# Optimization experiments

Measured on AMD Instinct MI355X. Metric: run time of the kernel, lower is better.

Reference implementation:

```python
import jax, jax.numpy as jnp
from jax import lax
import numpy as np

PARAM_SPECS = [
    ("w1", (16, 15, 5, 5)), ("b1", (16,)),
    ("w2", (32, 16, 3, 3)), ("b2", (32,)),
    ("w3", (32, 32, 3, 3)), ("b3", (32,)),
    ("w4", (32, 32, 3, 3)), ("b4", (32,)),
    ("w5", (64, 32, 3, 3)), ("b5", (64,)),
    ("w6", (32, 96, 3, 3)), ("b6", (32,)),
    ("w7", (32, 64, 3, 3)), ("b7", (32,)),
    ("w8", (32, 64, 3, 3)), ("b8", (32,)),
    ("w9", (64, 48, 3, 3)), ("b9", (64,)),
    ("wi", (16, 15, 3, 3)), ("bi", (16,)),
    ("wo", (3, 16, 3, 3)), ("bo", (3,)),
]


def conv2d(x, w, b, pad):
    y = lax.conv_general_dilated(x, w, (1, 1), [(pad, pad), (pad, pad)],
                                 dimension_numbers=("NCHW", "OIHW", "NCHW"))
    return y + b[None, :, None, None]


def maxpool2(x):
    return lax.reduce_window(x, -jnp.inf, lax.max, (1, 1, 2, 2), (1, 1, 2, 2), "VALID")


def upsample(x, hw):
    # bilinear, half-pixel centers == torch align_corners=False
    B, C = x.shape[:2]
    return jax.image.resize(x, (B, C, hw[0], hw[1]), method="bilinear")


def dcnn(img, p):
    x1 = jax.nn.relu(conv2d(img, p["w1"], p["b1"], 2))
    x2 = jax.nn.relu(conv2d(maxpool2(x1), p["w2"], p["b2"], 1))
    x3 = jax.nn.relu(conv2d(maxpool2(x2), p["w3"], p["b3"], 1))
    x4 = jax.nn.relu(conv2d(maxpool2(x3), p["w4"], p["b4"], 1))
    x5 = jax.nn.relu(conv2d(maxpool2(x4), p["w5"], p["b5"], 1))
    x6 = jax.nn.relu(conv2d(jnp.concatenate([upsample(x5, x4.shape[-2:]), x4], 1), p["w6"], p["b6"], 1))
    x7 = jax.nn.relu(conv2d(jnp.concatenate([upsample(x6, x3.shape[-2:]), x3], 1), p["w7"], p["b7"], 1))
    x8 = jax.nn.relu(conv2d(jnp.concatenate([upsample(x7, x2.shape[-2:]), x2], 1), p["w8"], p["b8"], 1))
    x9 = conv2d(jnp.concatenate([upsample(x8, x1.shape[-2:]), x1], 1), p["w9"], p["b9"], 1)
    return x9


def lrnn_op(X, P, axis, flip):
    # h_k = (1-P_k)*X_k + P_k*h_{k-1}, scanned along `axis`.
    # For reverse directions the torch code stacks hidden states in scan
    # order (spatially flipped) -> flip inputs, scan forward, keep order.
    if flip:
        X = jnp.flip(X, axis)
        P = jnp.flip(P, axis)
    xs = jnp.moveaxis(X, axis, 0)  # [L, B, 16, n]
    ps = jnp.moveaxis(P, axis, 0)

    def step(h, xp):
        x, p = xp
        h = (1.0 - p) * x + p * h
        return h, h

    h0 = jnp.zeros_like(xs[0])
    _, ys = lax.scan(step, h0, (xs, ps))
    return jnp.moveaxis(ys, 0, axis)


def lrnn_layer(x_in, fm):
    dirs = [(0, 3, False), (0, 3, True), (16, 2, False), (16, 2, True),
            (32, 3, False), (32, 3, True), (48, 2, False), (48, 2, True)]
    outs = [lrnn_op(x_in, fm[:, c:c + 16], axis, flip) for (c, axis, flip) in dirs]
    return jnp.max(jnp.stack(outs, axis=1), axis=1)


def setup_inputs() -> dict:
    key = jax.random.key(0)
    ks = jax.random.split(key, len(PARAM_SPECS) + 1)
    inp = {"img": jax.random.normal(ks[0], (8, 15, 256, 256), jnp.float32)}
    for i, (name, shape) in enumerate(PARAM_SPECS):
        inp[name] = jax.random.normal(ks[i + 1], shape, jnp.float32) * 0.05
    return inp


def reference(img, w1, b1, w2, b2, w3, b3, w4, b4, w5, b5, w6, b6, w7, b7,
              w8, b8, w9, b9, wi, bi, wo, bo):
    p = dict(w1=w1, b1=b1, w2=w2, b2=b2, w3=w3, b3=b3, w4=w4, b4=b4, w5=w5,
             b5=b5, w6=w6, b6=b6, w7=w7, b7=b7, w8=w8, b8=b8, w9=w9, b9=b9)
    fm = jnp.tanh(dcnn(img, p))          # [B,64,H,W]
    x_in = conv2d(img, wi, bi, 1)         # [B,16,H,W]
    out = lrnn_layer(x_in, fm)            # [B,16,H,W]
    return jax.nn.sigmoid(conv2d(out, wo, bo, 1))  # [B,3,H,W]
```

## Files before the change

### kernel.cpp

```cpp
#include <hip/hip_runtime.h>
#include <math.h>

typedef __attribute__((ext_vector_type(8)))  short bf16x8;
typedef __attribute__((ext_vector_type(8)))  unsigned short u16x8;
typedef __attribute__((ext_vector_type(16))) float f32x16;

__device__ __forceinline__ unsigned short f2bf(float f) {
    unsigned u = __float_as_uint(f);
    unsigned r = (u + 0x7FFFu + ((u >> 16) & 1u)) >> 16;
    return (unsigned short)r;
}
__device__ __forceinline__ float bf2f(unsigned short h) {
    return __uint_as_float(((unsigned)h) << 16);
}
__device__ __forceinline__ unsigned pack2(unsigned short a, unsigned short b) {
    return (unsigned)a | ((unsigned)b << 16);
}
__device__ __forceinline__ float fast_tanh(float x) {
    float e = __expf(2.f * x);
    return 1.f - 2.f / (e + 1.f);
}

__device__ __forceinline__ void bilin_setup(int y, int x, int Hi, int Wi,
                                            int& i00, int& i01, int& i10, int& i11,
                                            float& wy, float& wx)
{
    float fy = 0.5f * y - 0.25f;
    float fx = 0.5f * x - 0.25f;
    float y0f = floorf(fy), x0f = floorf(fx);
    wy = fy - y0f; wx = fx - x0f;
    int yA = (int)y0f, xA = (int)x0f;
    int yB = yA + 1, xB = xA + 1;
    yA = yA < 0 ? 0 : (yA > Hi - 1 ? Hi - 1 : yA);
    yB = yB < 0 ? 0 : (yB > Hi - 1 ? Hi - 1 : yB);
    xA = xA < 0 ? 0 : (xA > Wi - 1 ? Wi - 1 : xA);
    xB = xB < 0 ? 0 : (xB > Wi - 1 ? Wi - 1 : xB);
    i00 = yA * Wi + xA; i01 = yA * Wi + xB;
    i10 = yB * Wi + xA; i11 = yB * Wi + xB;
}

__global__ void upcat_nhwc2(const unsigned short* __restrict__ up,
                            const unsigned short* __restrict__ skip,
                            unsigned short* __restrict__ dst,
                            int C1, int C2, int H, int W)
{
    int C8 = (C1 + C2) >> 3;
    int idx = blockIdx.x * 256 + threadIdx.x;
    int total = 8 * H * W * C8;
    if (idx >= total) return;
    int g = idx % C8;
    int p = idx / C8;
    int x = p % W;
    int y = (p / W) % H;
    int b = p / (W * H);
    u16x8 r;
    if (g < (C1 >> 3)) {
        int Hi = H >> 1, Wi = W >> 1;
        int i00, i01, i10, i11; float wy, wx;
        bilin_setup(y, x, Hi, Wi, i00, i01, i10, i11, wy, wx);
        const unsigned short* sb = up + (size_t)b * Hi * Wi * C1 + g * 8;
        u16x8 v00 = *(const u16x8*)(sb + (size_t)i00 * C1);
        u16x8 v01 = *(const u16x8*)(sb + (size_t)i01 * C1);
        u16x8 v10 = *(const u16x8*)(sb + (size_t)i10 * C1);
        u16x8 v11 = *(const u16x8*)(sb + (size_t)i11 * C1);
        float w00 = (1.f - wy) * (1.f - wx), w01 = (1.f - wy) * wx;
        float w10 = wy * (1.f - wx),         w11 = wy * wx;
#pragma unroll
        for (int j = 0; j < 8; ++j)
            r[j] = f2bf(w00 * bf2f(v00[j]) + w01 * bf2f(v01[j]) +
                        w10 * bf2f(v10[j]) + w11 * bf2f(v11[j]));
    } else {
        r = *(const u16x8*)(skip + ((size_t)(b * H + y) * W + x) * C2 + (g - (C1 >> 3)) * 8);
    }
    *(u16x8*)(dst + (((size_t)(b * H + y) * W + x) * (C1 + C2) + g * 8)) = r;
}

__global__ void upx8_kernel(const unsigned short* __restrict__ x8t,
                            unsigned short* __restrict__ x8u)
{
    int idx = blockIdx.x * 256 + threadIdx.x;
    if (idx >= 8 * 256 * 256 * 4) return;
    int g = idx & 3;
    int p = idx >> 2;
    int x = p & 255, y = (p >> 8) & 255, b = p >> 16;
    int i00, i01, i10, i11; float wy, wx;
    bilin_setup(y, x, 128, 128, i00, i01, i10, i11, wy, wx);
    const unsigned short* sb = x8t + (size_t)b * 128 * 128 * 32 + g * 8;
    u16x8 v00 = *(const u16x8*)(sb + (size_t)i00 * 32);
    u16x8 v01 = *(const u16x8*)(sb + (size_t)i01 * 32);
    u16x8 v10 = *(const u16x8*)(sb + (size_t)i10 * 32);
    u16x8 v11 = *(const u16x8*)(sb + (size_t)i11 * 32);
    float w00 = (1.f - wy) * (1.f - wx), w01 = (1.f - wy) * wx;
    float w10 = wy * (1.f - wx),         w11 = wy * wx;
    u16x8 r;
#pragma unroll
    for (int j = 0; j < 8; ++j)
        r[j] = f2bf(w00 * bf2f(v00[j]) + w01 * bf2f(v01[j]) +
                    w10 * bf2f(v10[j]) + w11 * bf2f(v11[j]));
    *(u16x8*)(x8u + (size_t)idx * 8) = r;
}

__global__ void imgT_bf16(const float* __restrict__ img, unsigned short* __restrict__ dst)
{
    int idx = blockIdx.x * 256 + threadIdx.x;
    if (idx >= 8 * 256 * 256) return;
    int x = idx & 255, y = (idx >> 8) & 255, b = idx >> 16;
    unsigned short v[16];
#pragma unroll
    for (int c = 0; c < 15; ++c)
        v[c] = f2bf(img[(size_t)(b * 15 + c) * 65536 + y * 256 + x]);
    v[15] = 0;
    uint4 lo = make_uint4(pack2(v[0], v[1]), pack2(v[2], v[3]), pack2(v[4], v[5]), pack2(v[6], v[7]));
    uint4 hi = make_uint4(pack2(v[8], v[9]), pack2(v[10], v[11]), pack2(v[12], v[13]), pack2(v[14], v[15]));
    *(uint4*)(dst + (size_t)idx * 16)     = lo;
    *(uint4*)(dst + (size_t)idx * 16 + 8) = hi;
}

__device__ __forceinline__ void pack33(const float* __restrict__ w,
                                       unsigned short* __restrict__ dst,
                                       int i, int Cin, int Cout)
{
    int KST = Cin >> 4, MT = Cout >> 5;
    int j = i & 7;
    int lane = (i >> 3) & 63;
    int t = i >> 9;
    int mt = t % MT; t /= MT;
    int kst = t % KST;
    int s = t / KST;
    int oc = mt * 32 + (lane & 31);
    int ci = kst * 16 + (lane >> 5) * 8 + j;
    dst[i] = f2bf(w[(oc * Cin + ci) * 9 + s]);
}

__global__ void wprep_mega(const float* __restrict__ w9, const float* __restrict__ w8,
                           const float* __restrict__ w1, const float* __restrict__ wi,
                           const float* __restrict__ wo, const float* __restrict__ w2,
                           const float* __restrict__ w3, const float* __restrict__ w4,
                           const float* __restrict__ w5, const float* __restrict__ w6,
                           const float* __restrict__ w7,
                           unsigned short* __restrict__ wpk9, unsigned short* __restrict__ wpk8,
                           unsigned short* __restrict__ wpk1, unsigned short* __restrict__ wpki,
                           unsigned short* __restrict__ wpko, unsigned short* __restrict__ wpk2,
                           unsigned short* __restrict__ wpk3, unsigned short* __restrict__ wpk4,
                           unsigned short* __restrict__ wpk5, unsigned short* __restrict__ wpk6,
                           unsigned short* __restrict__ wpk7)
{
    int idx = blockIdx.x * 256 + threadIdx.x;
    if (idx < 27648)       pack33(w9, wpk9, idx, 48, 64);
    else if (idx < 46080)  pack33(w8, wpk8, idx - 27648, 64, 32);
    else if (idx < 58880) {
        int i = idx - 46080;
        int j = i & 7;
        int lane = (i >> 3) & 63;
        int s = i >> 9;
        int oc = lane & 31;
        int ci = (lane >> 5) * 8 + j;
        float v = 0.f;
        if (oc < 16 && ci < 15) v = w1[((oc * 15 + ci) * 5 + s / 5) * 5 + s % 5];
        wpk1[i] = f2bf(v);
    } else if (idx < 63488) {
        int i = idx - 58880;
        int j = i & 7;
        int lane = (i >> 3) & 63;
        int s = i >> 9;
        int oc = lane & 31;
        int ci = (lane >> 5) * 8 + j;
        float v = 0.f;
        if (oc < 16 && ci < 15) v = wi[((oc * 15 + ci) * 3 + s / 3) * 3 + s % 3];
        wpki[i] = f2bf(v);
    } else if (idx < 68096) {
        int i = idx - 63488;
        int j = i & 7;
        int lane = (i >> 3) & 63;
        int s = i >> 9;
        int oc = lane & 31;
        int ci = (lane >> 5) * 8 + j;
        float v = 0.f;
        if (oc < 3) v = wo[((oc * 16 + ci) * 3 + s / 3) * 3 + s % 3];
        wpko[i] = f2bf(v);
    }
    else if (idx < 72704)  pack33(w2, wpk2, idx - 68096, 16, 32);
    else if (idx < 81920)  pack33(w3, wpk3, idx - 72704, 32, 32);
    else if (idx < 91136)  pack33(w4, wpk4, idx - 81920, 32, 32);
    else if (idx < 109568) pack33(w5, wpk5, idx - 91136, 32, 64);
    else if (idx < 137216) pack33(w6, wpk6, idx - 109568, 96, 32);
    else if (idx < 155648) pack33(w7, wpk7, idx - 137216, 64, 32);
}

template<int CIN, int COUT, int H, int W, int ROWS, int POOL>
__global__ __launch_bounds__(256)
void convN_mfma(const unsigned short* __restrict__ in,
                const unsigned short* __restrict__ wpk,
                const float* __restrict__ bias,
                unsigned short* __restrict__ out)
{
    constexpr int G = CIN / 8;
    constexpr int KST = CIN / 16;
    constexpr int MT = COUT / 32;
    constexpr int TR = ROWS + 2;
    constexpr int TWd = W + 2;
    constexpr int PS = TR * TWd * 8 + 8;
    __shared__ __align__(16) unsigned short smem[G * PS];

    const int tid  = threadIdx.x;
    const int lane = tid & 63;
    const int wv   = tid >> 6;
    const int q    = lane >> 5;
    const int y0   = blockIdx.x * ROWS;
    const int b    = blockIdx.y;

    for (int i = tid; i < G * TR * TWd; i += 256) {
        int g = i % G;
        int u = (i / G) % TWd;
        int t = i / (G * TWd);
        int yg = y0 + t - 1, xg = u - 1;
        u16x8 v = {0, 0, 0, 0, 0, 0, 0, 0};
        if (yg >= 0 && yg < H && xg >= 0 && xg < W) {
            if (POOL) {
                const unsigned short* q0 =
                    in + (((size_t)(b * 2 * H + 2 * yg) * 2 * W + 2 * xg) * CIN + g * 8);
                u16x8 a0 = *(const u16x8*)q0;
                u16x8 a1 = *(const u16x8*)(q0 + CIN);
                u16x8 a2 = *(const u16x8*)(q0 + (size_t)2 * W * CIN);
                u16x8 a3 = *(const u16x8*)(q0 + (size_t)2 * W * CIN + CIN);
#pragma unroll
                for (int j = 0; j < 8; ++j)
                    v[j] = f2bf(fmaxf(fmaxf(bf2f(a0[j]), bf2f(a1[j])),
                                      fmaxf(bf2f(a2[j]), bf2f(a3[j]))));
            } else {
                v = *(const u16x8*)(in + (((size_t)(b * H + yg) * W + xg) * CIN + g * 8));
            }
        }
        *(u16x8*)(&smem[g * PS + (t * TWd + u) * 8]) = v;
    }
    __syncthreads();

    const int p = wv * 32 + (lane & 31);
    const int r = p / W;
    const int x = p % W;

    f32x16 acc[MT];
#pragma unroll
    for (int mt = 0; mt < MT; ++mt)
#pragma unroll
        for (int i = 0; i < 16; ++i) acc[mt][i] = 0.f;

    const unsigned short* wbase = wpk + lane * 8;

#pragma unroll
    for (int s = 0; s < 9; ++s) {
        const int dy = s / 3, dx = s % 3;
#pragma unroll
        for (int kst = 0; kst < KST; ++kst) {
            const int g = kst * 2 + q;
            bf16x8 bfrag = *(const bf16x8*)(&smem[g * PS + ((r + dy) * TWd + (x + dx)) * 8]);
#pragma unroll
            for (int mt = 0; mt < MT; ++mt) {
                bf16x8 a = *(const bf16x8*)(wbase + ((s * KST + kst) * MT + mt) * 512);
                acc[mt] = __builtin_amdgcn_mfma_f32_32x32x16_bf16(a, bfrag, acc[mt], 0, 0, 0);
            }
        }
    }

    size_t base = ((size_t)(b * H + y0 + r) * W + x) * COUT;
#pragma unroll
    for (int mt = 0; mt < MT; ++mt)
#pragma unroll
        for (int rg = 0; rg < 4; ++rg) {
            int oc = mt * 32 + 8 * rg + 4 * q;
            unsigned short s0 = f2bf(fmaxf(acc[mt][rg * 4 + 0] + bias[oc + 0], 0.f));
            unsigned short s1 = f2bf(fmaxf(acc[mt][rg * 4 + 1] + bias[oc + 1], 0.f));
            unsigned short s2 = f2bf(fmaxf(acc[mt][rg * 4 + 2] + bias[oc + 2], 0.f));
            unsigned short s3 = f2bf(fmaxf(acc[mt][rg * 4 + 3] + bias[oc + 3], 0.f));
            *(uint2*)(out + base + oc) = make_uint2(pack2(s0, s1), pack2(s2, s3));
        }
}

__global__ __launch_bounds__(256)
void conv1i_mfma(const unsigned short* __restrict__ imgT,
                 const unsigned short* __restrict__ wpk1,
                 const unsigned short* __restrict__ wpki,
                 const float* __restrict__ b1, const float* __restrict__ bi,
                 unsigned short* __restrict__ x1t, unsigned short* __restrict__ xin)
{
    __shared__ __align__(16) unsigned short smem[2 * 5 * 132 * 8];

    const int tid  = threadIdx.x;
    const int lane = tid & 63;
    const int wv   = tid >> 6;
    const int n    = lane & 31;
    const int q    = lane >> 5;
    const int y    = blockIdx.x >> 1;
    const int x0   = (blockIdx.x & 1) * 128;
    const int b    = blockIdx.y;

    for (int i = tid; i < 5 * 132 * 2; i += 256) {
        int r   = i / 264;
        int rem = i - r * 264;
        int xi  = rem >> 1;
        int g   = rem & 1;
        int yg = y + r - 2;
        int xg = x0 - 2 + xi;
        uint4 v = make_uint4(0, 0, 0, 0);
        if (yg >= 0 && yg < 256 && xg >= 0 && xg < 256)
            v = *(const uint4*)(imgT + (((size_t)(b * 256 + yg) * 256 + xg) * 16 + g * 8));
        *(uint4*)(&smem[((g * 5 + r) * 132 + xi) * 8]) = v;
    }
    __syncthreads();

    f32x16 acc1, acci;
#pragma unroll
    for (int i = 0; i < 16; ++i) { acc1[i] = 0.f; acci[i] = 0.f; }

    const int pxl = wv * 32 + n;
    const unsigned short* wb1 = wpk1 + lane * 8;
    const unsigned short* wbi = wpki + lane * 8;

#pragma unroll
    for (int s = 0; s < 25; ++s) {
        const int dy = s / 5, dx = s % 5;
        bf16x8 bfrag = *(const bf16x8*)(&smem[((q * 5 + dy) * 132 + pxl + dx) * 8]);
        bf16x8 a = *(const bf16x8*)(wb1 + s * 512);
        acc1 = __builtin_amdgcn_mfma_f32_32x32x16_bf16(a, bfrag, acc1, 0, 0, 0);
    }
#pragma unroll
    for (int s = 0; s < 9; ++s) {
        const int dy = s / 3, dx = s % 3;
        bf16x8 bfrag = *(const bf16x8*)(&smem[((q * 5 + dy + 1) * 132 + pxl + dx + 1) * 8]);
        bf16x8 a = *(const bf16x8*)(wbi + s * 512);
        acci = __builtin_amdgcn_mfma_f32_32x32x16_bf16(a, bfrag, acci, 0, 0, 0);
    }

    const int px = x0 + pxl;
    size_t base1 = ((size_t)(b * 256 + y) * 256 + px) * 16;
#pragma unroll
    for (int rg = 0; rg < 2; ++rg) {
        int oc = 8 * rg + 4 * q;
        unsigned short s0 = f2bf(fmaxf(acc1[rg * 4 + 0] + b1[oc + 0], 0.f));
        unsigned short s1 = f2bf(fmaxf(acc1[rg * 4 + 1] + b1[oc + 1], 0.f));
        unsigned short s2 = f2bf(fmaxf(acc1[rg * 4 + 2] + b1[oc + 2], 0.f));
        unsigned short s3 = f2bf(fmaxf(acc1[rg * 4 + 3] + b1[oc + 3], 0.f));
        *(uint2*)(x1t + base1 + oc) = make_uint2(pack2(s0, s1), pack2(s2, s3));
    }
#pragma unroll
    for (int reg = 0; reg < 8; ++reg) {
        int row = (reg & 3) + 8 * (reg >> 2) + 4 * q;
        xin[((size_t)(b * 16 + row) * 256 + y) * 256 + px] = f2bf(acci[reg] + bi[row]);
    }
}

__global__ __launch_bounds__(256)
void conv8_mfma(const unsigned short* __restrict__ cat8t,
                const unsigned short* __restrict__ wpk8,
                const float* __restrict__ bias,
                unsigned short* __restrict__ x8t)
{
    __shared__ __align__(16) unsigned short smem[8 * 3 * 130 * 8];

    const int tid  = threadIdx.x;
    const int lane = tid & 63;
    const int wv   = tid >> 6;
    const int n    = lane & 31;
    const int q    = lane >> 5;
    const int y    = blockIdx.x;
    const int b    = blockIdx.y;

    for (int i = tid; i < 3 * 130 * 8; i += 256) {
        int r   = i / 1040;
        int rem = i - r * 1040;
        int xi  = rem >> 3;
        int g   = rem & 7;
        int yg = y + r - 1;
        int xg = xi - 1;
        uint4 v = make_uint4(0, 0, 0, 0);
        if (yg >= 0 && yg < 128 && xg >= 0 && xg < 128)
            v = *(const uint4*)(cat8t + (((size_t)(b * 128 + yg) * 128 + xg) * 64 + g * 8));
        *(uint4*)(&smem[((g * 3 + r) * 130 + xi) * 8]) = v;
    }
    __syncthreads();

    f32x16 acc;
#pragma unroll
    for (int i = 0; i < 16; ++i) acc[i] = 0.f;

    const int pxl = wv * 32 + n;
    const unsigned short* wbase = wpk8 + lane * 8;

#pragma unroll
    for (int s = 0; s < 9; ++s) {
        const int dy = s / 3, dx = s % 3;
        const int xi = pxl + dx;
#pragma unroll
        for (int kst = 0; kst < 4; ++kst) {
            const int g = kst * 2 + q;
            bf16x8 bfrag = *(const bf16x8*)(&smem[((g * 3 + dy) * 130 + xi) * 8]);
            bf16x8 a = *(const bf16x8*)(wbase + (s * 4 + kst) * 512);
            acc = __builtin_amdgcn_mfma_f32_32x32x16_bf16(a, bfrag, acc, 0, 0, 0);
        }
    }

    size_t base = ((size_t)(b * 128 + y) * 128 + pxl) * 32;
#pragma unroll
    for (int rg = 0; rg < 4; ++rg) {
        int oc0 = 8 * rg + 4 * q;
        unsigned short s0 = f2bf(fmaxf(acc[rg * 4 + 0] + bias[oc0 + 0], 0.f));
        unsigned short s1 = f2bf(fmaxf(acc[rg * 4 + 1] + bias[oc0 + 1], 0.f));
        unsigned short s2 = f2bf(fmaxf(acc[rg * 4 + 2] + bias[oc0 + 2], 0.f));
        unsigned short s3 = f2bf(fmaxf(acc[rg * 4 + 3] + bias[oc0 + 3], 0.f));
        *(uint2*)(x8t + base + oc0) = make_uint2(pack2(s0, s1), pack2(s2, s3));
    }
}

__global__ __launch_bounds__(256)
void conv9f_mfma(const unsigned short* __restrict__ x8u,
                 const unsigned short* __restrict__ x1t,
                 const unsigned short* __restrict__ wpk,
                 const float* __restrict__ bias,
                 unsigned short* __restrict__ fm)
{
    __shared__ __align__(16) unsigned short smem[6 * 3 * 130 * 8];

    const int tid  = threadIdx.x;
    const int lane = tid & 63;
    const int wv   = tid >> 6;
    const int n    = lane & 31;
    const int q    = lane >> 5;
    const int y    = blockIdx.x >> 1;
    const int x0   = (blockIdx.x & 1) * 128;
    const int b    = blockIdx.y;

    for (int i = tid; i < 3 * 130 * 6; i += 256) {
        int r   = i / 780;
        int rem = i - r * 780;
        int xi  = rem / 6;
        int g   = rem - xi * 6;
        int yg = y + r - 1;
        int xg = x0 - 1 + xi;
        uint4 v = make_uint4(0, 0, 0, 0);
        if (yg >= 0 && yg < 256 && xg >= 0 && xg < 256) {
            if (g < 4)
                v = *(const uint4*)(x8u + (((size_t)(b * 256 + yg) * 256 + xg) * 32 + g * 8));
            else
                v = *(const uint4*)(x1t + (((size_t)(b * 256 + yg) * 256 + xg) * 16 + (g - 4) * 8));
        }
        *(uint4*)(&smem[((g * 3 + r) * 130 + xi) * 8]) = v;
    }
    __syncthreads();

    f32x16 acc0, acc1;
#pragma unroll
    for (int i = 0; i < 16; ++i) { acc0[i] = 0.f; acc1[i] = 0.f; }

    const int pxl = wv * 32 + n;
    const unsigned short* wbase = wpk + lane * 8;

#pragma unroll
    for (int s = 0; s < 9; ++s) {
        const int dy = s / 3, dx = s % 3;
        const int xi = pxl + dx;
#pragma unroll
        for (int kst = 0; kst < 3; ++kst) {
            const int g = kst * 2 + q;
            bf16x8 bfrag = *(const bf16x8*)(&smem[((g * 3 + dy) * 130 + xi) * 8]);
            bf16x8 a0 = *(const bf16x8*)(wbase + ((s * 3 + kst) * 2 + 0) * 512);
            bf16x8 a1 = *(const bf16x8*)(wbase + ((s * 3 + kst) * 2 + 1) * 512);
            acc0 = __builtin_amdgcn_mfma_f32_32x32x16_bf16(a0, bfrag, acc0, 0, 0, 0);
            acc1 = __builtin_amdgcn_mfma_f32_32x32x16_bf16(a1, bfrag, acc1, 0, 0, 0);
        }
    }

    const int px = x0 + pxl;
#pragma unroll
    for (int reg = 0; reg < 16; ++reg) {
        int row = (reg & 3) + 8 * (reg >> 2) + 4 * q;
        int oc0 = row, oc1 = 32 + row;
        fm[(((size_t)b * 64 + oc0) * 256 + y) * 256 + px] = f2bf(fast_tanh(acc0[reg] + bias[oc0]));
        fm[(((size_t)b * 64 + oc1) * 256 + y) * 256 + px] = f2bf(fast_tanh(acc1[reg] + bias[oc1]));
    }
}

__device__ __forceinline__ int X2C(int x) { return x + (x >> 5); }

__global__ __launch_bounds__(256)
void lrnn_w_seg(const unsigned short* __restrict__ X, const unsigned short* __restrict__ FM,
                unsigned short* __restrict__ rnnW)
{
    __shared__ float tx[3][16][264];
    __shared__ unsigned short outm[2][16][256];
    __shared__ float segres[2][16][8][4];
    __shared__ float hin[2][16][8][2];

    const int tid = threadIdx.x;
    const int bid = blockIdx.x;
    const int yt = bid & 15;
    const int c  = (bid >> 4) & 15;
    const int b  = bid >> 8;
    const int y0 = yt * 16;

    const size_t xb  = ((size_t)(b * 16 + c) * 256 + y0) * 256;
    const size_t p1b = ((size_t)(b * 64 + c) * 256 + y0) * 256;
    const size_t p2b = ((size_t)(b * 64 + 32 + c) * 256 + y0) * 256;

    for (int i = tid; i < 1536; i += 256) {
        int s = i >> 9;
        int r = i & 511;
        int y = r >> 5;
        int g = r & 31;
        const unsigned short* sp = (s == 0) ? (X + xb) : (s == 1 ? FM + p1b : FM + p2b);
        u16x8 v = *(const u16x8*)(sp + (size_t)y * 256 + g * 8);
        int c0 = X2C(g * 8);
#pragma unroll
        for (int j = 0; j < 8; ++j) tx[s][y][c0 + j] = bf2f(v[j]);
    }
    __syncthreads();

    const int y  = tid & 15;
    const int sg = (tid >> 4) & 7;
    const int d  = tid >> 7;

    {
        float h1 = 0.f, h2 = 0.f, A1 = 1.f, A2 = 1.f;
        if (d == 0) {
            int cs = X2C(sg * 32);
#pragma unroll
            for (int i = 0; i < 32; ++i) {
                float xv = tx[0][y][cs + i], p1 = tx[1][y][cs + i], p2 = tx[2][y][cs + i];
                h1 = fmaf(p1, h1 - xv, xv); A1 *= p1;
                h2 = fmaf(p2, h2 - xv, xv); A2 *= p2;
            }
        } else {
            int cs = X2C(255 - sg * 32);
#pragma unroll
            for (int i = 0; i < 32; ++i) {
                float xv = tx[0][y][cs - i], p1 = tx[1][y][cs - i], p2 = tx[2][y][cs - i];
                h1 = fmaf(p1, h1 - xv, xv); A1 *= p1;
                h2 = fmaf(p2, h2 - xv, xv); A2 *= p2;
            }
        }
        segres[d][y][sg][0] = h1; segres[d][y][sg][1] = A1;
        segres[d][y][sg][2] = h2; segres[d][y][sg][3] = A2;
    }
    __syncthreads();

    if (tid < 32) {
        int yy = tid & 15, dd = tid >> 4;
        float c1 = 0.f, c2 = 0.f;
        for (int s = 0; s < 8; ++s) {
            hin[dd][yy][s][0] = c1;
            hin[dd][yy][s][1] = c2;
            c1 = segres[dd][yy][s][0] + segres[dd][yy][s][1] * c1;
            c2 = segres[dd][yy][s][2] + segres[dd][yy][s][3] * c2;
        }
    }
    __syncthreads();

    {
        float h1 = hin[d][y][sg][0], h2 = hin[d][y][sg][1];
        if (d == 0) {
            int cs = X2C(sg * 32);
            int xs = sg * 32;
#pragma unroll
            for (int i = 0; i < 32; ++i) {
                float xv = tx[0][y][cs + i], p1 = tx[1][y][cs + i], p2 = tx[2][y][cs + i];
                h1 = fmaf(p1, h1 - xv, xv);
                h2 = fmaf(p2, h2 - xv, xv);
                outm[0][y][xs + i] = f2bf(fmaxf(h1, h2));
            }
        } else {
            int cs = X2C(255 - sg * 32);
#pragma unroll
            for (int i = 0; i < 32; ++i) {
                int t = sg * 32 + i;
                float xv = tx[0][y][cs - i], p1 = tx[1][y][cs - i], p2 = tx[2][y][cs - i];
                h1 = fmaf(p1, h1 - xv, xv);
                h2 = fmaf(p2, h2 - xv, xv);
                outm[1][y][t] = f2bf(fmaxf(h1, h2));
            }
        }
    }
    __syncthreads();

    for (int i = tid; i < 4096; i += 256) {
        int x = i & 255, yy = i >> 8;
        float m = fmaxf(bf2f(outm[0][yy][x]), bf2f(outm[1][yy][x]));
        rnnW[xb + (size_t)yy * 256 + x] = f2bf(m);
    }
}

__global__ __launch_bounds__(256)
void lrnn_h_seg(const unsigned short* __restrict__ X, const unsigned short* __restrict__ FM,
                unsigned short* __restrict__ rnnH)
{
    __shared__ float tx[3][264][17];
    __shared__ unsigned short outm[2][256][16];
    __shared__ float segres[2][16][8][4];
    __shared__ float hin[2][16][8][2];

    const int tid = threadIdx.x;
    const int bid = blockIdx.x;
    const int xt = bid & 15;
    const int c  = (bid >> 4) & 15;
    const int b  = bid >> 8;
    const int x0 = xt * 16;

    const size_t xb  = (size_t)(b * 16 + c) * 65536 + x0;
    const size_t p1b = (size_t)(b * 64 + 16 + c) * 65536 + x0;
    const size_t p2b = (size_t)(b * 64 + 48 + c) * 65536 + x0;

    for (int i = tid; i < 1536; i += 256) {
        int s = i >> 9;
        int r = i & 511;
        int y = r >> 1;
        int g = r & 1;
        const unsigned short* sp = (s == 0) ? (X + xb) : (s == 1 ? FM + p1b : FM + p2b);
        u16x8 v = *(const u16x8*)(sp + (size_t)y * 256 + g * 8);
        int pr = y + (y >> 5);
#pragma unroll
        for (int j = 0; j < 8; ++j) tx[s][pr][g * 8 + j] = bf2f(v[j]);
    }
    __syncthreads();

    const int x  = tid & 15;
    const int sg = (tid >> 4) & 7;
    const int d  = tid >> 7;

    {
        float h1 = 0.f, h2 = 0.f, A1 = 1.f, A2 = 1.f;
        if (d == 0) {
            int rs = X2C(sg * 32);
#pragma unroll
            for (int i = 0; i < 32; ++i) {
                float xv = tx[0][rs + i][x], p1 = tx[1][rs + i][x], p2 = tx[2][rs + i][x];
                h1 = fmaf(p1, h1 - xv, xv); A1 *= p1;
                h2 = fmaf(p2, h2 - xv, xv); A2 *= p2;
            }
        } else {
            int rs = X2C(255 - sg * 32);
#pragma unroll
            for (int i = 0; i < 32; ++i) {
                float xv = tx[0][rs - i][x], p1 = tx[1][rs - i][x], p2 = tx[2][rs - i][x];
                h1 = fmaf(p1, h1 - xv, xv); A1 *= p1;
                h2 = fmaf(p2, h2 - xv, xv); A2 *= p2;
            }
        }
        segres[d][x][sg][0] = h1; segres[d][x][sg][1] = A1;
        segres[d][x][sg][2] = h2; segres[d][x][sg][3] = A2;
    }
    __syncthreads();

    if (tid < 32) {
        int xx = tid & 15, dd = tid >> 4;
        float c1 = 0.f, c2 = 0.f;
        for (int s = 0; s < 8; ++s) {
            hin[dd][xx][s][0] = c1;
            hin[dd][xx][s][1] = c2;
            c1 = segres[dd][xx][s][0] + segres[dd][xx][s][1] * c1;
            c2 = segres[dd][xx][s][2] + segres[dd][xx][s][3] * c2;
        }
    }
    __syncthreads();

    {
        float h1 = hin[d][x][sg][0], h2 = hin[d][x][sg][1];
        if (d == 0) {
            int rs = X2C(sg * 32);
            int ys = sg * 32;
#pragma unroll
            for (int i = 0; i < 32; ++i) {
                float xv = tx[0][rs + i][x], p1 = tx[1][rs + i][x], p2 = tx[2][rs + i][x];
                h1 = fmaf(p1, h1 - xv, xv);
                h2 = fmaf(p2, h2 - xv, xv);
                outm[0][ys + i][x] = f2bf(fmaxf(h1, h2));
            }
        } else {
            int rs = X2C(255 - sg * 32);
#pragma unroll
            for (int i = 0; i < 32; ++i) {
                int t = sg * 32 + i;
                float xv = tx[0][rs - i][x], p1 = tx[1][rs - i][x], p2 = tx[2][rs - i][x];
                h1 = fmaf(p1, h1 - xv, xv);
                h2 = fmaf(p2, h2 - xv, xv);
                outm[1][t][x] = f2bf(fmaxf(h1, h2));
            }
        }
    }
    __syncthreads();

    for (int i = tid; i < 4096; i += 256) {
        int xx = i & 15, yy = i >> 4;
        float m = fmaxf(bf2f(outm[0][yy][xx]), bf2f(outm[1][yy][xx]));
        rnnH[xb + (size_t)yy * 256 + xx] = f2bf(m);
    }
}

__global__ __launch_bounds__(256)
void convo_mfma(const unsigned short* __restrict__ rnnW,
                const unsigned short* __restrict__ rnnH,
                const unsigned short* __restrict__ wpko,
                const float* __restrict__ bo,
                float* __restrict__ outp)
{
    __shared__ __align__(16) unsigned short smem[2 * 3 * 130 * 8];

    const int tid  = threadIdx.x;
    const int lane = tid & 63;
    const int wv   = tid >> 6;
    const int n    = lane & 31;
    const int q    = lane >> 5;
    const int y    = blockIdx.x >> 1;
    const int x0   = (blockIdx.x & 1) * 128;
    const int b    = blockIdx.y;

    for (int i = tid; i < 3 * 16 * 130; i += 256) {
        int xi = i % 130;
        int t  = i / 130;
        int ch = t & 15;
        int r  = t >> 4;
        int yg = y + r - 1;
        int xg = x0 - 1 + xi;
        unsigned short m = 0;
        if (yg >= 0 && yg < 256 && xg >= 0 && xg < 256) {
            size_t off = (size_t)(b * 16 + ch) * 65536 + yg * 256 + xg;
            m = f2bf(fmaxf(bf2f(rnnW[off]), bf2f(rnnH[off])));
        }
        int g = ch >> 3, j = ch & 7;
        smem[((g * 3 + r) * 130 + xi) * 8 + j] = m;
    }
    __syncthreads();

    f32x16 acc;
#pragma unroll
    for (int i = 0; i < 16; ++i) acc[i] = 0.f;

    const int pxl = wv * 32 + n;
    const unsigned short* wbase = wpko + lane * 8;

#pragma unroll
    for (int s = 0; s < 9; ++s) {
        const int dy = s / 3, dx = s % 3;
        bf16x8 bfrag = *(const bf16x8*)(&smem[((q * 3 + dy) * 130 + pxl + dx) * 8]);
        bf16x8 a = *(const bf16x8*)(wbase + s * 512);
        acc = __builtin_amdgcn_mfma_f32_32x32x16_bf16(a, bfrag, acc, 0, 0, 0);
    }

    const int px = x0 + pxl;
    if (q == 0) {
#pragma unroll
        for (int oc = 0; oc < 3; ++oc) {
            float r = acc[oc] + bo[oc];
            outp[((size_t)(b * 3 + oc) * 256 + y) * 256 + px] = 1.f / (1.f + __expf(-r));
        }
    }
}

extern "C" void kernel_launch(void* const* d_in, const int* in_sizes, int n_in,
                              void* d_out, int out_size, void* d_ws, size_t ws_size,
                              hipStream_t stream)
{
    const float* img = (const float*)d_in[0];
    const float* w1 = (const float*)d_in[1];  const float* b1 = (const float*)d_in[2];
    const float* w2 = (const float*)d_in[3];  const float* b2 = (const float*)d_in[4];
    const float* w3 = (const float*)d_in[5];  const float* b3 = (const float*)d_in[6];
    const float* w4 = (const float*)d_in[7];  const float* b4 = (const float*)d_in[8];
    const float* w5 = (const float*)d_in[9];  const float* b5 = (const float*)d_in[10];
    const float* w6 = (const float*)d_in[11]; const float* b6 = (const float*)d_in[12];
    const float* w7 = (const float*)d_in[13]; const float* b7 = (const float*)d_in[14];
    const float* w8 = (const float*)d_in[15]; const float* b8 = (const float*)d_in[16];
    const float* w9 = (const float*)d_in[17]; const float* b9 = (const float*)d_in[18];
    const float* wi = (const float*)d_in[19]; const float* bi = (const float*)d_in[20];
    const float* wo = (const float*)d_in[21]; const float* bo = (const float*)d_in[22];

    char* wsb = (char*)d_ws;
    const size_t MB = (size_t)(1u << 20);
    unsigned short* imgT  = (unsigned short*)(wsb);
    unsigned short* x1t   = (unsigned short*)(wsb + 16 * MB);
    unsigned short* x2t   = (unsigned short*)(wsb + 32 * MB);
    unsigned short* x3t   = (unsigned short*)(wsb + 40 * MB);
    unsigned short* x4t   = (unsigned short*)(wsb + 42 * MB);
    unsigned short* x5t   = (unsigned short*)(wsb + 43 * MB);
    unsigned short* cat6t = (unsigned short*)(wsb + 44 * MB);
    unsigned short* x6t   = (unsigned short*)(wsb + 46 * MB);
    unsigned short* cat7t = (unsigned short*)(wsb + 47 * MB);
    unsigned short* x7t   = (unsigned short*)(wsb + 51 * MB);
    unsigned short* cat8t = (unsigned short*)(wsb + 54 * MB);
    unsigned short* x8t   = (unsigned short*)(wsb + 70 * MB);
    unsigned short* x8u   = (unsigned short*)(wsb + 78 * MB);
    unsigned short* fm16  = (unsigned short*)(wsb + 112 * MB);
    unsigned short* xin16 = (unsigned short*)(wsb + 176 * MB);
    unsigned short* rnnW  = (unsigned short*)(wsb);
    unsigned short* rnnH  = (unsigned short*)(wsb + 16 * MB);
    unsigned short* wpk9 = (unsigned short*)(wsb + 192 * MB);
    unsigned short* wpk8 = wpk9 + 27648;
    unsigned short* wpk1 = wpk8 + 18432;
    unsigned short* wpki = wpk1 + 12800;
    unsigned short* wpko = wpki + 4608;
    unsigned short* wpk2 = wpko + 4608;
    unsigned short* wpk3 = wpk2 + 4608;
    unsigned short* wpk4 = wpk3 + 9216;
    unsigned short* wpk5 = wpk4 + 9216;
    unsigned short* wpk6 = wpk5 + 18432;
    unsigned short* wpk7 = wpk6 + 27648;
    float* outp = (float*)d_out;

    wprep_mega<<<608, 256, 0, stream>>>(w9, w8, w1, wi, wo, w2, w3, w4, w5, w6, w7,
                                        wpk9, wpk8, wpk1, wpki, wpko,
                                        wpk2, wpk3, wpk4, wpk5, wpk6, wpk7);
    imgT_bf16<<<2048, 256, 0, stream>>>(img, imgT);

    { dim3 grd(512, 8);
      conv1i_mfma<<<grd, 256, 0, stream>>>(imgT, wpk1, wpki, b1, bi, x1t, xin16); }

    convN_mfma<16, 32, 128, 128, 1, 1><<<dim3(128, 8), 256, 0, stream>>>(x1t, wpk2, b2, x2t);
    convN_mfma<32, 32, 64, 64, 2, 1><<<dim3(32, 8), 256, 0, stream>>>(x2t, wpk3, b3, x3t);
    convN_mfma<32, 32, 32, 32, 4, 1><<<dim3(8, 8), 256, 0, stream>>>(x3t, wpk4, b4, x4t);
    convN_mfma<32, 64, 16, 16, 8, 1><<<dim3(2, 8), 256, 0, stream>>>(x4t, wpk5, b5, x5t);

    upcat_nhwc2<<<384, 256, 0, stream>>>(x5t, x4t, cat6t, 64, 32, 32, 32);
    convN_mfma<96, 32, 32, 32, 4, 0><<<dim3(8, 8), 256, 0, stream>>>(cat6t, wpk6, b6, x6t);
    upcat_nhwc2<<<1024, 256, 0, stream>>>(x6t, x3t, cat7t, 32, 32, 64, 64);
    convN_mfma<64, 32, 64, 64, 2, 0><<<dim3(32, 8), 256, 0, stream>>>(cat7t, wpk7, b7, x7t);
    upcat_nhwc2<<<4096, 256, 0, stream>>>(x7t, x2t, cat8t, 32, 32, 128, 128);
    { dim3 grd(128, 8);
      conv8_mfma<<<grd, 256, 0, stream>>>(cat8t, wpk8, b8, x8t); }

    upx8_kernel<<<8192, 256, 0, stream>>>(x8t, x8u);
    { dim3 grd(512, 8);
      conv9f_mfma<<<grd, 256, 0, stream>>>(x8u, x1t, wpk9, b9, fm16); }

    lrnn_w_seg<<<2048, 256, 0, stream>>>(xin16, fm16, rnnW);
    lrnn_h_seg<<<2048, 256, 0, stream>>>(xin16, fm16, rnnH);

    { dim3 grd(512, 8);
      convo_mfma<<<grd, 256, 0, stream>>>(rnnW, rnnH, wpko, bo, outp); }
}
```

Before: 418.1 us.

## Fuse upsample-concat into conv6/conv7 and retile conv8/conv9 as 2-row blocks

```diff
diff --git a/kernel.cpp b/kernel.cpp
--- a/kernel.cpp
+++ b/kernel.cpp
@@ -37,6 +37,24 @@
     xB = xB < 0 ? 0 : (xB > Wi - 1 ? Wi - 1 : xB);
     i00 = yA * Wi + xA; i01 = yA * Wi + xB;
     i10 = yB * Wi + xA; i11 = yB * Wi + xB;
+}
+
+__device__ __forceinline__ u16x8 bilin8(const unsigned short* __restrict__ sb,
+                                        int i00, int i01, int i10, int i11,
+                                        float wy, float wx, int stride)
+{
+    u16x8 v00 = *(const u16x8*)(sb + (size_t)i00 * stride);
+    u16x8 v01 = *(const u16x8*)(sb + (size_t)i01 * stride);
+    u16x8 v10 = *(const u16x8*)(sb + (size_t)i10 * stride);
+    u16x8 v11 = *(const u16x8*)(sb + (size_t)i11 * stride);
+    float w00 = (1.f - wy) * (1.f - wx), w01 = (1.f - wy) * wx;
+    float w10 = wy * (1.f - wx),         w11 = wy * wx;
+    u16x8 r;
+#pragma unroll
+    for (int j = 0; j < 8; ++j)
+        r[j] = f2bf(w00 * bf2f(v00[j]) + w01 * bf2f(v01[j]) +
+                    w10 * bf2f(v10[j]) + w11 * bf2f(v11[j]));
+    return r;
 }
 
 __global__ void upcat_nhwc2(const unsigned short* __restrict__ up,
@@ -58,17 +76,7 @@
         int Hi = H >> 1, Wi = W >> 1;
         int i00, i01, i10, i11; float wy, wx;
         bilin_setup(y, x, Hi, Wi, i00, i01, i10, i11, wy, wx);
-        const unsigned short* sb = up + (size_t)b * Hi * Wi * C1 + g * 8;
-        u16x8 v00 = *(const u16x8*)(sb + (size_t)i00 * C1);
-        u16x8 v01 = *(const u16x8*)(sb + (size_t)i01 * C1);
-        u16x8 v10 = *(const u16x8*)(sb + (size_t)i10 * C1);
-        u16x8 v11 = *(const u16x8*)(sb + (size_t)i11 * C1);
-        float w00 = (1.f - wy) * (1.f - wx), w01 = (1.f - wy) * wx;
-        float w10 = wy * (1.f - wx),         w11 = wy * wx;
-#pragma unroll
-        for (int j = 0; j < 8; ++j)
-            r[j] = f2bf(w00 * bf2f(v00[j]) + w01 * bf2f(v01[j]) +
-                        w10 * bf2f(v10[j]) + w11 * bf2f(v11[j]));
+        r = bilin8(up + (size_t)b * Hi * Wi * C1 + g * 8, i00, i01, i10, i11, wy, wx, C1);
     } else {
         r = *(const u16x8*)(skip + ((size_t)(b * H + y) * W + x) * C2 + (g - (C1 >> 3)) * 8);
     }
@@ -85,18 +93,7 @@
     int x = p & 255, y = (p >> 8) & 255, b = p >> 16;
     int i00, i01, i10, i11; float wy, wx;
     bilin_setup(y, x, 128, 128, i00, i01, i10, i11, wy, wx);
-    const unsigned short* sb = x8t + (size_t)b * 128 * 128 * 32 + g * 8;
-    u16x8 v00 = *(const u16x8*)(sb + (size_t)i00 * 32);
-    u16x8 v01 = *(const u16x8*)(sb + (size_t)i01 * 32);
-    u16x8 v10 = *(const u16x8*)(sb + (size_t)i10 * 32);
-    u16x8 v11 = *(const u16x8*)(sb + (size_t)i11 * 32);
-    float w00 = (1.f - wy) * (1.f - wx), w01 = (1.f - wy) * wx;
-    float w10 = wy * (1.f - wx),         w11 = wy * wx;
-    u16x8 r;
-#pragma unroll
-    for (int j = 0; j < 8; ++j)
-        r[j] = f2bf(w00 * bf2f(v00[j]) + w01 * bf2f(v01[j]) +
-                    w10 * bf2f(v10[j]) + w11 * bf2f(v11[j]));
+    u16x8 r = bilin8(x8t + (size_t)b * 128 * 128 * 32 + g * 8, i00, i01, i10, i11, wy, wx, 32);
     *(u16x8*)(x8u + (size_t)idx * 8) = r;
 }
 
@@ -276,6 +273,93 @@
         }
 }
 
+template<int UPC, int CSKIP, int COUT, int H, int W, int ROWS>
+__global__ __launch_bounds__(256)
+void convU_mfma(const unsigned short* __restrict__ up,
+                const unsigned short* __restrict__ skip,
+                const unsigned short* __restrict__ wpk,
+                const float* __restrict__ bias,
+                unsigned short* __restrict__ out)
+{
+    constexpr int CIN = UPC + CSKIP;
+    constexpr int G = CIN / 8;
+    constexpr int GU = UPC / 8;
+    constexpr int KST = CIN / 16;
+    constexpr int MT = COUT / 32;
+    constexpr int TR = ROWS + 2;
+    constexpr int TWd = W + 2;
+    constexpr int PS = TR * TWd * 8 + 8;
+    __shared__ __align__(16) unsigned short smem[G * PS];
+
+    const int tid  = threadIdx.x;
+    const int lane = tid & 63;
+    const int wv   = tid >> 6;
+    const int q    = lane >> 5;
+    const int y0   = blockIdx.x * ROWS;
+    const int b    = blockIdx.y;
+
+    for (int i = tid; i < G * TR * TWd; i += 256) {
+        int g = i % G;
+        int u = (i / G) % TWd;
+        int t = i / (G * TWd);
+        int yg = y0 + t - 1, xg = u - 1;
+        u16x8 v = {0, 0, 0, 0, 0, 0, 0, 0};
+        if (yg >= 0 && yg < H && xg >= 0 && xg < W) {
+            if (g < GU) {
+                int i00, i01, i10, i11; float wy, wx;
+                bilin_setup(yg, xg, H / 2, W / 2, i00, i01, i10, i11, wy, wx);
+                v = bilin8(up + (size_t)b * (H / 2) * (W / 2) * UPC + g * 8,
+                           i00, i01, i10, i11, wy, wx, UPC);
+            } else {
+                v = *(const u16x8*)(skip + (((size_t)(b * H + yg) * W + xg) * CSKIP
+                                            + (g - GU) * 8));
+            }
+        }
+        *(u16x8*)(&smem[g * PS + (t * TWd + u) * 8]) = v;
+    }
+    __syncthreads();
+
+    const int p = wv * 32 + (lane & 31);
+    const int r = p / W;
+    const int x = p % W;
+
+    f32x16 acc[MT];
+#pragma unroll
+    for (int mt = 0; mt < MT; ++mt)
+#pragma unroll
+        for (int i = 0; i < 16; ++i) acc[mt][i] = 0.f;
+
+    const unsigned short* wbase = wpk + lane * 8;
+
+#pragma unroll
+    for (int s = 0; s < 9; ++s) {
+        const int dy = s / 3, dx = s % 3;
+#pragma unroll
+        for (int kst = 0; kst < KST; ++kst) {
+            const int g = kst * 2 + q;
+            bf16x8 bfrag = *(const bf16x8*)(&smem[g * PS + ((r + dy) * TWd + (x + dx)) * 8]);
+#pragma unroll
+            for (int mt = 0; mt < MT; ++mt) {
+                bf16x8 a = *(const bf16x8*)(wbase + ((s * KST + kst) * MT + mt) * 512);
+                acc[mt] = __builtin_amdgcn_mfma_f32_32x32x16_bf16(a, bfrag, acc[mt], 0, 0, 0);
+            }
+        }
+    }
+
+    size_t base = ((size_t)(b * H + y0 + r) * W + x) * COUT;
+#pragma unroll
+    for (int mt = 0; mt < MT; ++mt)
+#pragma unroll
+        for (int rg = 0; rg < 4; ++rg) {
+            int oc = mt * 32 + 8 * rg + 4 * q;
+            unsigned short s0 = f2bf(fmaxf(acc[mt][rg * 4 + 0] + bias[oc + 0], 0.f));
+            unsigned short s1 = f2bf(fmaxf(acc[mt][rg * 4 + 1] + bias[oc + 1], 0.f));
+            unsigned short s2 = f2bf(fmaxf(acc[mt][rg * 4 + 2] + bias[oc + 2], 0.f));
+            unsigned short s3 = f2bf(fmaxf(acc[mt][rg * 4 + 3] + bias[oc + 3], 0.f));
+            *(uint2*)(out + base + oc) = make_uint2(pack2(s0, s1), pack2(s2, s3));
+        }
+}
+
 __global__ __launch_bounds__(256)
 void conv1i_mfma(const unsigned short* __restrict__ imgT,
                  const unsigned short* __restrict__ wpk1,
@@ -355,51 +439,53 @@
                 const float* __restrict__ bias,
                 unsigned short* __restrict__ x8t)
 {
-    __shared__ __align__(16) unsigned short smem[8 * 3 * 130 * 8];
+    __shared__ __align__(16) unsigned short smem[8 * 4 * 66 * 8];
 
     const int tid  = threadIdx.x;
     const int lane = tid & 63;
     const int wv   = tid >> 6;
     const int n    = lane & 31;
     const int q    = lane >> 5;
-    const int y    = blockIdx.x;
+    const int x0   = (blockIdx.x & 1) * 64;
+    const int yp   = blockIdx.x >> 1;
     const int b    = blockIdx.y;
 
-    for (int i = tid; i < 3 * 130 * 8; i += 256) {
-        int r   = i / 1040;
-        int rem = i - r * 1040;
+    for (int i = tid; i < 8 * 4 * 66; i += 256) {
+        int t   = i / 528;
+        int rem = i - t * 528;
         int xi  = rem >> 3;
         int g   = rem & 7;
-        int yg = y + r - 1;
-        int xg = xi - 1;
+        int yg = 2 * yp + t - 1;
+        int xg = x0 - 1 + xi;
         uint4 v = make_uint4(0, 0, 0, 0);
         if (yg >= 0 && yg < 128 && xg >= 0 && xg < 128)
             v = *(const uint4*)(cat8t + (((size_t)(b * 128 + yg) * 128 + xg) * 64 + g * 8));
-        *(uint4*)(&smem[((g * 3 + r) * 130 + xi) * 8]) = v;
-    }
-    __syncthreads();
+        *(uint4*)(&smem[((g * 4 + t) * 66 + xi) * 8]) = v;
+    }
+    __syncthreads();
+
+    const int rr  = wv >> 1;
+    const int pxl = (wv & 1) * 32 + n;
 
     f32x16 acc;
 #pragma unroll
     for (int i = 0; i < 16; ++i) acc[i] = 0.f;
 
-    const int pxl = wv * 32 + n;
     const unsigned short* wbase = wpk8 + lane * 8;
 
 #pragma unroll
     for (int s = 0; s < 9; ++s) {
         const int dy = s / 3, dx = s % 3;
-        const int xi = pxl + dx;
 #pragma unroll
         for (int kst = 0; kst < 4; ++kst) {
             const int g = kst * 2 + q;
-            bf16x8 bfrag = *(const bf16x8*)(&smem[((g * 3 + dy) * 130 + xi) * 8]);
+            bf16x8 bfrag = *(const bf16x8*)(&smem[((g * 4 + rr + dy) * 66 + pxl + dx) * 8]);
             bf16x8 a = *(const bf16x8*)(wbase + (s * 4 + kst) * 512);
             acc = __builtin_amdgcn_mfma_f32_32x32x16_bf16(a, bfrag, acc, 0, 0, 0);
         }
     }
 
-    size_t base = ((size_t)(b * 128 + y) * 128 + pxl) * 32;
+    size_t base = ((size_t)(b * 128 + 2 * yp + rr) * 128 + x0 + pxl) * 32;
 #pragma unroll
     for (int rg = 0; rg < 4; ++rg) {
         int oc0 = 8 * rg + 4 * q;
@@ -418,23 +504,23 @@
                  const float* __restrict__ bias,
                  unsigned short* __restrict__ fm)
 {
-    __shared__ __align__(16) unsigned short smem[6 * 3 * 130 * 8];
+    __shared__ __align__(16) unsigned short smem[6 * 4 * 66 * 8];
 
     const int tid  = threadIdx.x;
     const int lane = tid & 63;
     const int wv   = tid >> 6;
     const int n    = lane & 31;
     const int q    = lane >> 5;
-    const int y    = blockIdx.x >> 1;
-    const int x0   = (blockIdx.x & 1) * 128;
+    const int x0   = (blockIdx.x & 3) * 64;
+    const int yp   = blockIdx.x >> 2;
     const int b    = blockIdx.y;
 
-    for (int i = tid; i < 3 * 130 * 6; i += 256) {
-        int r   = i / 780;
-        int rem = i - r * 780;
+    for (int i = tid; i < 6 * 4 * 66; i += 256) {
+        int t   = i / 396;
+        int rem = i - t * 396;
         int xi  = rem / 6;
         int g   = rem - xi * 6;
-        int yg = y + r - 1;
+        int yg = 2 * yp + t - 1;
         int xg = x0 - 1 + xi;
         uint4 v = make_uint4(0, 0, 0, 0);
         if (yg >= 0 && yg < 256 && xg >= 0 && xg < 256) {
@@ -443,25 +529,26 @@
             else
                 v = *(const uint4*)(x1t + (((size_t)(b * 256 + yg) * 256 + xg) * 16 + (g - 4) * 8));
         }
-        *(uint4*)(&smem[((g * 3 + r) * 130 + xi) * 8]) = v;
-    }
-    __syncthreads();
+        *(uint4*)(&smem[((g * 4 + t) * 66 + xi) * 8]) = v;
+    }
+    __syncthreads();
+
+    const int rr  = wv >> 1;
+    const int pxl = (wv & 1) * 32 + n;
 
     f32x16 acc0, acc1;
 #pragma unroll
     for (int i = 0; i < 16; ++i) { acc0[i] = 0.f; acc1[i] = 0.f; }
 
-    const int pxl = wv * 32 + n;
     const unsigned short* wbase = wpk + lane * 8;
 
 #pragma unroll
     for (int s = 0; s < 9; ++s) {
         const int dy = s / 3, dx = s % 3;
-        const int xi = pxl + dx;
 #pragma unroll
         for (int kst = 0; kst < 3; ++kst) {
             const int g = kst * 2 + q;
-            bf16x8 bfrag = *(const bf16x8*)(&smem[((g * 3 + dy) * 130 + xi) * 8]);
+            bf16x8 bfrag = *(const bf16x8*)(&smem[((g * 4 + rr + dy) * 66 + pxl + dx) * 8]);
             bf16x8 a0 = *(const bf16x8*)(wbase + ((s * 3 + kst) * 2 + 0) * 512);
             bf16x8 a1 = *(const bf16x8*)(wbase + ((s * 3 + kst) * 2 + 1) * 512);
             acc0 = __builtin_amdgcn_mfma_f32_32x32x16_bf16(a0, bfrag, acc0, 0, 0, 0);
@@ -469,6 +556,7 @@
         }
     }
 
+    const int y  = 2 * yp + rr;
     const int px = x0 + pxl;
 #pragma unroll
     for (int reg = 0; reg < 16; ++reg) {
@@ -778,9 +866,7 @@
     unsigned short* x3t   = (unsigned short*)(wsb + 40 * MB);
     unsigned short* x4t   = (unsigned short*)(wsb + 42 * MB);
     unsigned short* x5t   = (unsigned short*)(wsb + 43 * MB);
-    unsigned short* cat6t = (unsigned short*)(wsb + 44 * MB);
     unsigned short* x6t   = (unsigned short*)(wsb + 46 * MB);
-    unsigned short* cat7t = (unsigned short*)(wsb + 47 * MB);
     unsigned short* x7t   = (unsigned short*)(wsb + 51 * MB);
     unsigned short* cat8t = (unsigned short*)(wsb + 54 * MB);
     unsigned short* x8t   = (unsigned short*)(wsb + 70 * MB);
@@ -815,10 +901,8 @@
     convN_mfma<32, 32, 32, 32, 4, 1><<<dim3(8, 8), 256, 0, stream>>>(x3t, wpk4, b4, x4t);
     convN_mfma<32, 64, 16, 16, 8, 1><<<dim3(2, 8), 256, 0, stream>>>(x4t, wpk5, b5, x5t);
 
-    upcat_nhwc2<<<384, 256, 0, stream>>>(x5t, x4t, cat6t, 64, 32, 32, 32);
-    convN_mfma<96, 32, 32, 32, 4, 0><<<dim3(8, 8), 256, 0, stream>>>(cat6t, wpk6, b6, x6t);
-    upcat_nhwc2<<<1024, 256, 0, stream>>>(x6t, x3t, cat7t, 32, 32, 64, 64);
-    convN_mfma<64, 32, 64, 64, 2, 0><<<dim3(32, 8), 256, 0, stream>>>(cat7t, wpk7, b7, x7t);
+    convU_mfma<64, 32, 32, 32, 32, 4><<<dim3(8, 8), 256, 0, stream>>>(x5t, x4t, wpk6, b6, x6t);
+    convU_mfma<32, 32, 32, 64, 64, 2><<<dim3(32, 8), 256, 0, stream>>>(x6t, x3t, wpk7, b7, x7t);
     upcat_nhwc2<<<4096, 256, 0, stream>>>(x7t, x2t, cat8t, 32, 32, 128, 128);
     { dim3 grd(128, 8);
       conv8_mfma<<<grd, 256, 0, stream>>>(cat8t, wpk8, b8, x8t); }
```

New measurement: 407.2 us. 2.6% less time.
